# Optimization experiments

Measured on AMD Instinct MI355X. Metric: run time of the kernel, lower is better.

Reference implementation:

```python
import jax, jax.numpy as jnp
import numpy as np

N = 50000
E = 800000
IN_C, HID, OUT_C = 512, 256, 128


def gcn_conv(x, edge_index, W, b, num_nodes):
    # PyG GCNConv: add self-loops, symmetric normalization, linear-then-aggregate.
    h = x @ W  # [N, out]
    src = jnp.concatenate([edge_index[0], jnp.arange(num_nodes)])
    dst = jnp.concatenate([edge_index[1], jnp.arange(num_nodes)])
    ones = jnp.ones(src.shape[0], dtype=x.dtype)
    deg = jax.ops.segment_sum(ones, dst, num_segments=num_nodes)  # in-degree incl. self-loop
    dinv = jax.lax.rsqrt(deg)  # deg >= 1 thanks to self-loops
    norm = dinv[src] * dinv[dst]  # [E+N]
    msg = h[src] * norm[:, None]  # gather + scale
    out = jax.ops.segment_sum(msg, dst, num_segments=num_nodes)  # scatter-add
    return out + b


def setup_inputs() -> dict:
    key = jax.random.key(0)
    k_x, k_e, k_w1, k_b1, k_w2, k_b2 = jax.random.split(key, 6)
    x = jax.random.normal(k_x, (N, IN_C), dtype=jnp.float32)
    edge_index = jax.random.randint(k_e, (2, E), 0, N, dtype=jnp.int64)
    s1 = 1.0 / np.sqrt(IN_C)
    s2 = 1.0 / np.sqrt(HID)
    W1 = jax.random.uniform(k_w1, (IN_C, HID), jnp.float32, -s1, s1)
    b1 = jax.random.uniform(k_b1, (HID,), jnp.float32, -s1, s1)
    W2 = jax.random.uniform(k_w2, (HID, OUT_C), jnp.float32, -s2, s2)
    b2 = jax.random.uniform(k_b2, (OUT_C,), jnp.float32, -s2, s2)
    return {"x": x, "edge_index": edge_index, "W1": W1, "b1": b1, "W2": W2, "b2": b2}


def reference(x, edge_index, W1, b1, W2, b2):
    h = gcn_conv(x, edge_index, W1, b1, N)
    h = jax.nn.relu(h)
    # dropout in eval mode == identity
    return gcn_conv(h, edge_index, W2, b2, N)
```

## Files before the change

### kernel.cpp

```cpp
#include <hip/hip_runtime.h>
#include <stdint.h>

typedef __bf16 bf16_t;
typedef bf16_t bf16x8 __attribute__((ext_vector_type(8)));
typedef bf16_t bf16x4 __attribute__((ext_vector_type(4)));
typedef bf16_t bf16x2 __attribute__((ext_vector_type(2)));
typedef float  f32x4  __attribute__((ext_vector_type(4)));

#define IN_C 512
#define HID  256
#define OUTC 128

__global__ void k_detect(const void* __restrict__ ei, int* __restrict__ flag, int n_nodes) {
  if (blockIdx.x == 0 && threadIdx.x == 0) {
    const long long* p = (const long long*)ei;
    int ok = 1;
    for (int i = 0; i < 64; ++i) {
      long long v = p[i];
      if (v < 0 || v >= n_nodes) ok = 0;
    }
    *flag = ok;
  }
}

__global__ void k_decode_hist(const void* __restrict__ ei, const int* __restrict__ flag,
                              int* __restrict__ srcI, int* __restrict__ dstI,
                              int* __restrict__ cnt, int E) {
  int e = blockIdx.x * blockDim.x + threadIdx.x;
  if (e >= E) return;
  int s, d;
  if (*flag) {
    const long long* p = (const long long*)ei;
    s = (int)p[e];
    d = (int)p[(size_t)E + e];
  } else {
    const int* p = (const int*)ei;
    s = p[e];
    d = p[E + e];
  }
  srcI[e] = s;
  dstI[e] = d;
  atomicAdd(&cnt[d], 1);
}

__global__ void k_dinv(const int* __restrict__ cnt, float* __restrict__ dinv, int n) {
  int i = blockIdx.x * blockDim.x + threadIdx.x;
  if (i < n) dinv[i] = rsqrtf((float)cnt[i] + 1.0f);
}

__global__ void k_scan1(const int* __restrict__ cnt, int* __restrict__ ex,
                        int* __restrict__ part, int n) {
  __shared__ int sh[256];
  int i = blockIdx.x * 256 + threadIdx.x;
  int v = (i < n) ? cnt[i] : 0;
  sh[threadIdx.x] = v;
  __syncthreads();
  int val = v;
  for (int off = 1; off < 256; off <<= 1) {
    int t = (threadIdx.x >= off) ? sh[threadIdx.x - off] : 0;
    __syncthreads();
    val += t;
    sh[threadIdx.x] = val;
    __syncthreads();
  }
  if (i < n) ex[i] = val - v;
  if (threadIdx.x == 255) part[blockIdx.x] = val;
}

__global__ void k_scan2(int* __restrict__ part, int nb) {
  __shared__ int sh[256];
  int v = (threadIdx.x < nb) ? part[threadIdx.x] : 0;
  sh[threadIdx.x] = v;
  __syncthreads();
  int val = v;
  for (int off = 1; off < 256; off <<= 1) {
    int t = (threadIdx.x >= off) ? sh[threadIdx.x - off] : 0;
    __syncthreads();
    val += t;
    sh[threadIdx.x] = val;
    __syncthreads();
  }
  if (threadIdx.x < nb) part[threadIdx.x] = val - v;
}

__global__ void k_scan3(int* __restrict__ rs, const int* __restrict__ part,
                        int* __restrict__ cur, int n, int Etot) {
  int i = blockIdx.x * 256 + threadIdx.x;
  if (i < n) {
    int r = rs[i] + part[blockIdx.x];
    rs[i] = r;
    cur[i] = r;
  }
  if (i == 0) rs[n] = Etot;
}

__global__ void k_fill(const int* __restrict__ srcI, const int* __restrict__ dstI,
                       int* __restrict__ cur, int* __restrict__ csr, int E) {
  int e = blockIdx.x * blockDim.x + threadIdx.x;
  if (e >= E) return;
  int p = atomicAdd(&cur[dstI[e]], 1);
  csr[p] = srcI[e];
}

__global__ void k_convx(const float* __restrict__ x, bf16_t* __restrict__ Xb,
                        int n, int mpad) {
  int t = blockIdx.x * blockDim.x + threadIdx.x;
  int r = t >> 6, c8 = t & 63;
  if (r >= mpad) return;
  bf16x8 o;
  if (r < n) {
    const float4* px = (const float4*)(x + (size_t)r * IN_C);
    float4 a = px[c8 * 2];
    float4 b = px[c8 * 2 + 1];
    o[0] = (bf16_t)a.x; o[1] = (bf16_t)a.y; o[2] = (bf16_t)a.z; o[3] = (bf16_t)a.w;
    o[4] = (bf16_t)b.x; o[5] = (bf16_t)b.y; o[6] = (bf16_t)b.z; o[7] = (bf16_t)b.w;
  } else {
    for (int i = 0; i < 8; ++i) o[i] = (bf16_t)0.0f;
  }
  *(bf16x8*)(Xb + (size_t)r * IN_C + c8 * 8) = o;
}

__global__ void k_transpose(const float* __restrict__ W, bf16_t* __restrict__ Wt,
                            int K, int Ncols) {
  int t = blockIdx.x * blockDim.x + threadIdx.x;
  if (t >= K * Ncols) return;
  int k = t / Ncols, nn = t % Ncols;
  Wt[(size_t)nn * K + k] = (bf16_t)W[t];
}

__global__ __launch_bounds__(256, 2) void k_gemm(const bf16_t* __restrict__ A,
                                                 const bf16_t* __restrict__ Bt,
                                                 bf16_t* __restrict__ C,
                                                 int Kdim, int Ncols) {
  __shared__ bf16_t As[128 * 40];
  __shared__ bf16_t Bs[128 * 40];
  const int bm = blockIdx.x, bn = blockIdx.y;
  const int tid = threadIdx.x;
  const int wave = tid >> 6, lane = tid & 63;
  const int wm = (wave >> 1) * 64, wn = (wave & 1) * 64;
  const int quad = lane >> 4, l16 = lane & 15;
  const int seg = tid & 3;

  f32x4 acc[4][4];
  for (int i = 0; i < 4; ++i)
    for (int j = 0; j < 4; ++j)
      for (int r = 0; r < 4; ++r) acc[i][j][r] = 0.0f;

  for (int kk = 0; kk < Kdim; kk += 32) {
#pragma unroll
    for (int s = 0; s < 2; ++s) {
      int row = s * 64 + (tid >> 2);
      bf16x8 va = *(const bf16x8*)(A + (size_t)(bm * 128 + row) * Kdim + kk + seg * 8);
      *(bf16x8*)(&As[row * 40 + seg * 8]) = va;
      bf16x8 vb = *(const bf16x8*)(Bt + (size_t)(bn * 128 + row) * Kdim + kk + seg * 8);
      *(bf16x8*)(&Bs[row * 40 + seg * 8]) = vb;
    }
    __syncthreads();
    bf16x8 af[4], bfr[4];
#pragma unroll
    for (int i = 0; i < 4; ++i)
      af[i] = *(const bf16x8*)(&As[(wm + i * 16 + l16) * 40 + quad * 8]);
#pragma unroll
    for (int j = 0; j < 4; ++j)
      bfr[j] = *(const bf16x8*)(&Bs[(wn + j * 16 + l16) * 40 + quad * 8]);
#pragma unroll
    for (int i = 0; i < 4; ++i)
#pragma unroll
      for (int j = 0; j < 4; ++j)
        acc[i][j] = __builtin_amdgcn_mfma_f32_16x16x32_bf16(af[i], bfr[j], acc[i][j], 0, 0, 0);
    __syncthreads();
  }

#pragma unroll
  for (int i = 0; i < 4; ++i) {
#pragma unroll
    for (int j = 0; j < 4; ++j) {
      int col = bn * 128 + wn + j * 16 + l16;
      int row0 = bm * 128 + wm + i * 16 + quad * 4;
#pragma unroll
      for (int r = 0; r < 4; ++r)
        C[(size_t)(row0 + r) * Ncols + col] = (bf16_t)acc[i][j][r];
    }
  }
}

__global__ void k_agg_l1(const bf16_t* __restrict__ H, const int* __restrict__ rs,
                         const int* __restrict__ csr, const float* __restrict__ dinv,
                         const float* __restrict__ b1, bf16_t* __restrict__ R,
                         int n, int mpad) {
  int d = blockIdx.x * 4 + (threadIdx.x >> 6);
  if (d >= mpad) return;
  int lane = threadIdx.x & 63;
  if (d >= n) {
    bf16x4 z;
    z[0] = (bf16_t)0.0f; z[1] = (bf16_t)0.0f; z[2] = (bf16_t)0.0f; z[3] = (bf16_t)0.0f;
    *(bf16x4*)(R + (size_t)d * HID + lane * 4) = z;
    return;
  }
  int e0 = rs[d], e1 = rs[d + 1];
  float a0 = 0.f, a1 = 0.f, a2 = 0.f, a3 = 0.f;
  float c0 = 0.f, c1 = 0.f, c2 = 0.f, c3 = 0.f;
  int e = e0;
  for (; e + 2 <= e1; e += 2) {
    int s0 = csr[e], s1 = csr[e + 1];
    float w0 = dinv[s0], w1 = dinv[s1];
    bf16x4 h0 = *(const bf16x4*)(H + (size_t)s0 * HID + lane * 4);
    bf16x4 h1 = *(const bf16x4*)(H + (size_t)s1 * HID + lane * 4);
    a0 += w0 * (float)h0[0]; a1 += w0 * (float)h0[1];
    a2 += w0 * (float)h0[2]; a3 += w0 * (float)h0[3];
    c0 += w1 * (float)h1[0]; c1 += w1 * (float)h1[1];
    c2 += w1 * (float)h1[2]; c3 += w1 * (float)h1[3];
  }
  if (e < e1) {
    int s0 = csr[e];
    float w0 = dinv[s0];
    bf16x4 h0 = *(const bf16x4*)(H + (size_t)s0 * HID + lane * 4);
    a0 += w0 * (float)h0[0]; a1 += w0 * (float)h0[1];
    a2 += w0 * (float)h0[2]; a3 += w0 * (float)h0[3];
  }
  a0 += c0; a1 += c1; a2 += c2; a3 += c3;
  float dd = dinv[d];
  float dv2 = dd * dd;
  bf16x4 hs = *(const bf16x4*)(H + (size_t)d * HID + lane * 4);
  float4 bb = ((const float4*)b1)[lane];
  float v0 = fmaxf(a0 * dd + dv2 * (float)hs[0] + bb.x, 0.f);
  float v1 = fmaxf(a1 * dd + dv2 * (float)hs[1] + bb.y, 0.f);
  float v2 = fmaxf(a2 * dd + dv2 * (float)hs[2] + bb.z, 0.f);
  float v3 = fmaxf(a3 * dd + dv2 * (float)hs[3] + bb.w, 0.f);
  bf16x4 o;
  o[0] = (bf16_t)v0; o[1] = (bf16_t)v1; o[2] = (bf16_t)v2; o[3] = (bf16_t)v3;
  *(bf16x4*)(R + (size_t)d * HID + lane * 4) = o;
}

__global__ void k_agg_l2(const bf16_t* __restrict__ H, const int* __restrict__ rs,
                         const int* __restrict__ csr, const float* __restrict__ dinv,
                         const float* __restrict__ b2, float* __restrict__ out, int n) {
  int d = blockIdx.x * 4 + (threadIdx.x >> 6);
  if (d >= n) return;
  int lane = threadIdx.x & 63;
  int e0 = rs[d], e1 = rs[d + 1];
  float a0 = 0.f, a1 = 0.f, c0 = 0.f, c1 = 0.f;
  int e = e0;
  for (; e + 2 <= e1; e += 2) {
    int s0 = csr[e], s1 = csr[e + 1];
    float w0 = dinv[s0], w1 = dinv[s1];
    bf16x2 h0 = *(const bf16x2*)(H + (size_t)s0 * OUTC + lane * 2);
    bf16x2 h1 = *(const bf16x2*)(H + (size_t)s1 * OUTC + lane * 2);
    a0 += w0 * (float)h0[0]; a1 += w0 * (float)h0[1];
    c0 += w1 * (float)h1[0]; c1 += w1 * (float)h1[1];
  }
  if (e < e1) {
    int s0 = csr[e];
    float w0 = dinv[s0];
    bf16x2 h0 = *(const bf16x2*)(H + (size_t)s0 * OUTC + lane * 2);
    a0 += w0 * (float)h0[0]; a1 += w0 * (float)h0[1];
  }
  a0 += c0; a1 += c1;
  float dd = dinv[d];
  float dv2 = dd * dd;
  bf16x2 hs = *(const bf16x2*)(H + (size_t)d * OUTC + lane * 2);
  float2 bb = ((const float2*)b2)[lane];
  float2 o;
  o.x = a0 * dd + dv2 * (float)hs[0] + bb.x;
  o.y = a1 * dd + dv2 * (float)hs[1] + bb.y;
  ((float2*)(out + (size_t)d * OUTC))[lane] = o;
}

extern "C" void kernel_launch(void* const* d_in, const int* in_sizes, int n_in,
                              void* d_out, int out_size, void* d_ws, size_t ws_size,
                              hipStream_t stream) {
  const float* x  = (const float*)d_in[0];
  const void*  ei = d_in[1];
  const float* W1 = (const float*)d_in[2];
  const float* b1 = (const float*)d_in[3];
  const float* W2 = (const float*)d_in[4];
  const float* b2 = (const float*)d_in[5];

  const int n = in_sizes[0] / IN_C;
  const int E = in_sizes[1] / 2;
  const int mpad = (n + 127) & ~127;

  char* w = (char*)d_ws;
  size_t off = 0;
  auto alloc = [&](size_t bytes) -> void* {
    void* p = w + off;
    off = (off + bytes + 255) & ~(size_t)255;
    return p;
  };

  int*    flag = (int*)alloc(4);
  int*    srcI = (int*)alloc((size_t)E * 4);
  int*    dstI = (int*)alloc((size_t)E * 4);
  int*    cnt  = (int*)alloc((size_t)n * 4);
  float*  dinv = (float*)alloc((size_t)n * 4);
  int*    rs   = (int*)alloc((size_t)(n + 1) * 4);
  int*    cur  = (int*)alloc((size_t)n * 4);
  int*    part = (int*)alloc(1024);
  int*    csr  = (int*)alloc((size_t)E * 4);
  bf16_t* Xb   = (bf16_t*)alloc((size_t)mpad * IN_C * 2);
  bf16_t* W1t  = (bf16_t*)alloc((size_t)HID * IN_C * 2);
  bf16_t* H1b  = (bf16_t*)alloc((size_t)mpad * HID * 2);
  bf16_t* R1b  = (bf16_t*)alloc((size_t)mpad * HID * 2);
  bf16_t* W2t  = (bf16_t*)alloc((size_t)OUTC * HID * 2);
  bf16_t* H2b  = (bf16_t*)alloc((size_t)mpad * OUTC * 2);
  (void)ws_size; (void)n_in; (void)out_size;

  const int nb = (n + 255) / 256;

  hipMemsetAsync(cnt, 0, (size_t)n * 4, stream);
  k_detect<<<1, 64, 0, stream>>>(ei, flag, n);
  k_decode_hist<<<(E + 255) / 256, 256, 0, stream>>>(ei, flag, srcI, dstI, cnt, E);
  k_dinv<<<nb, 256, 0, stream>>>(cnt, dinv, n);
  k_scan1<<<nb, 256, 0, stream>>>(cnt, rs, part, n);
  k_scan2<<<1, 256, 0, stream>>>(part, nb);
  k_scan3<<<nb, 256, 0, stream>>>(rs, part, cur, n, E);
  k_fill<<<(E + 255) / 256, 256, 0, stream>>>(srcI, dstI, cur, csr, E);

  k_convx<<<(mpad * 64 + 255) / 256, 256, 0, stream>>>(x, Xb, n, mpad);
  k_transpose<<<(IN_C * HID + 255) / 256, 256, 0, stream>>>(W1, W1t, IN_C, HID);
  k_transpose<<<(HID * OUTC + 255) / 256, 256, 0, stream>>>(W2, W2t, HID, OUTC);

  k_gemm<<<dim3(mpad / 128, HID / 128), 256, 0, stream>>>(Xb, W1t, H1b, IN_C, HID);
  k_agg_l1<<<(mpad + 3) / 4, 256, 0, stream>>>(H1b, rs, csr, dinv, b1, R1b, n, mpad);
  k_gemm<<<dim3(mpad / 128, OUTC / 128), 256, 0, stream>>>(R1b, W2t, H2b, HID, OUTC);
  k_agg_l2<<<(n + 3) / 4, 256, 0, stream>>>(H2b, rs, csr, dinv, b2, (float*)d_out, n);
}
```

Baseline: 421.7 us.

## Fuse preprocessing kernels, store edge weights in CSR, unroll aggregation by eight

Merges the x conversion, both weight transposes, the count zeroing and the format detection into one prep kernel. The histogram kernel no longer writes decoded src/dst arrays, and the dinv computation moves into the first scan kernel. The fill kernel re-decodes edges and stores (src, dinv[src]) pairs, which removes the dependent dinv lookup during aggregation. Both aggregation kernels now issue eight gathers at once into four accumulator sets for more memory-level parallelism, at the cost of a larger CSR array and more registers.

```diff
diff --git a/kernel.cpp b/kernel.cpp
--- a/kernel.cpp
+++ b/kernel.cpp
@@ -11,21 +11,114 @@
 #define HID  256
 #define OUTC 128
 
-__global__ void k_detect(const void* __restrict__ ei, int* __restrict__ flag, int n_nodes) {
-  if (blockIdx.x == 0 && threadIdx.x == 0) {
+__global__ void k_prep(const float* __restrict__ x, const float* __restrict__ W1,
+                       const float* __restrict__ W2, const void* __restrict__ ei,
+                       int* __restrict__ flag, int* __restrict__ cnt,
+                       bf16_t* __restrict__ Xb, bf16_t* __restrict__ W1t,
+                       bf16_t* __restrict__ W2t, int n, int mpad) {
+  int t = blockIdx.x * blockDim.x + threadIdx.x;
+  const int NC = mpad * 64;
+  if (t < NC) {
+    int r = t >> 6, c8 = t & 63;
+    bf16x8 o;
+    if (r < n) {
+      const float4* px = (const float4*)(x + (size_t)r * IN_C);
+      float4 a = px[c8 * 2];
+      float4 b = px[c8 * 2 + 1];
+      o[0] = (bf16_t)a.x; o[1] = (bf16_t)a.y; o[2] = (bf16_t)a.z; o[3] = (bf16_t)a.w;
+      o[4] = (bf16_t)b.x; o[5] = (bf16_t)b.y; o[6] = (bf16_t)b.z; o[7] = (bf16_t)b.w;
+    } else {
+      for (int i = 0; i < 8; ++i) o[i] = (bf16_t)0.0f;
+    }
+    *(bf16x8*)(Xb + (size_t)r * IN_C + c8 * 8) = o;
+    return;
+  }
+  int u = t - NC;
+  if (u < IN_C * HID) {
+    W1t[(size_t)(u & 255) * IN_C + (u >> 8)] = (bf16_t)W1[u];
+    return;
+  }
+  u -= IN_C * HID;
+  if (u < HID * OUTC) {
+    W2t[(size_t)(u & 127) * HID + (u >> 7)] = (bf16_t)W2[u];
+    return;
+  }
+  u -= HID * OUTC;
+  if (u < n) {
+    cnt[u] = 0;
+    return;
+  }
+  if (u == n) {
     const long long* p = (const long long*)ei;
     int ok = 1;
     for (int i = 0; i < 64; ++i) {
       long long v = p[i];
-      if (v < 0 || v >= n_nodes) ok = 0;
+      if (v < 0 || v >= n) ok = 0;
     }
     *flag = ok;
   }
 }
 
-__global__ void k_decode_hist(const void* __restrict__ ei, const int* __restrict__ flag,
-                              int* __restrict__ srcI, int* __restrict__ dstI,
-                              int* __restrict__ cnt, int E) {
+__global__ void k_hist(const void* __restrict__ ei, const int* __restrict__ flag,
+                       int* __restrict__ cnt, int E) {
+  int e = blockIdx.x * blockDim.x + threadIdx.x;
+  if (e >= E) return;
+  int d;
+  if (*flag) d = (int)((const long long*)ei)[(size_t)E + e];
+  else       d = ((const int*)ei)[E + e];
+  atomicAdd(&cnt[d], 1);
+}
+
+__global__ void k_scan1(const int* __restrict__ cnt, int* __restrict__ ex,
+                        int* __restrict__ part, float* __restrict__ dinv, int n) {
+  __shared__ int sh[256];
+  int i = blockIdx.x * 256 + threadIdx.x;
+  int v = (i < n) ? cnt[i] : 0;
+  if (i < n) dinv[i] = rsqrtf((float)v + 1.0f);
+  sh[threadIdx.x] = v;
+  __syncthreads();
+  int val = v;
+  for (int off = 1; off < 256; off <<= 1) {
+    int t = (threadIdx.x >= off) ? sh[threadIdx.x - off] : 0;
+    __syncthreads();
+    val += t;
+    sh[threadIdx.x] = val;
+    __syncthreads();
+  }
+  if (i < n) ex[i] = val - v;
+  if (threadIdx.x == 255) part[blockIdx.x] = val;
+}
+
+__global__ void k_scan2(int* __restrict__ part, int nb) {
+  __shared__ int sh[256];
+  int v = (threadIdx.x < nb) ? part[threadIdx.x] : 0;
+  sh[threadIdx.x] = v;
+  __syncthreads();
+  int val = v;
+  for (int off = 1; off < 256; off <<= 1) {
+    int t = (threadIdx.x >= off) ? sh[threadIdx.x - off] : 0;
+    __syncthreads();
+    val += t;
+    sh[threadIdx.x] = val;
+    __syncthreads();
+  }
+  if (threadIdx.x < nb) part[threadIdx.x] = val - v;
+}
+
+__global__ void k_scan3(int* __restrict__ rs, const int* __restrict__ part,
+                        int* __restrict__ cur, int n, int Etot) {
+  int i = blockIdx.x * 256 + threadIdx.x;
+  if (i < n) {
+    int r = rs[i] + part[blockIdx.x];
+    rs[i] = r;
+    cur[i] = r;
+  }
+  if (i == 0) rs[n] = Etot;
+}
+
+__global__ void k_fill(const void* __restrict__ ei, const int* __restrict__ flag,
+                       int* __restrict__ cur, int2* __restrict__ csrw,
+                       const float* __restrict__ dinv, int E) {
   int e = blockIdx.x * blockDim.x + threadIdx.x;
   if (e >= E) return;
   int s, d;
@@ -38,94 +131,11 @@
     s = p[e];
     d = p[E + e];
   }
-  srcI[e] = s;
-  dstI[e] = d;
-  atomicAdd(&cnt[d], 1);
-}
-
-__global__ void k_dinv(const int* __restrict__ cnt, float* __restrict__ dinv, int n) {
-  int i = blockIdx.x * blockDim.x + threadIdx.x;
-  if (i < n) dinv[i] = rsqrtf((float)cnt[i] + 1.0f);
-}
-
-__global__ void k_scan1(const int* __restrict__ cnt, int* __restrict__ ex,
-                        int* __restrict__ part, int n) {
-  __shared__ int sh[256];
-  int i = blockIdx.x * 256 + threadIdx.x;
-  int v = (i < n) ? cnt[i] : 0;
-  sh[threadIdx.x] = v;
-  __syncthreads();
-  int val = v;
-  for (int off = 1; off < 256; off <<= 1) {
-    int t = (threadIdx.x >= off) ? sh[threadIdx.x - off] : 0;
-    __syncthreads();
-    val += t;
-    sh[threadIdx.x] = val;
-    __syncthreads();
-  }
-  if (i < n) ex[i] = val - v;
-  if (threadIdx.x == 255) part[blockIdx.x] = val;
-}
-
-__global__ void k_scan2(int* __restrict__ part, int nb) {
-  __shared__ int sh[256];
-  int v = (threadIdx.x < nb) ? part[threadIdx.x] : 0;
-  sh[threadIdx.x] = v;
-  __syncthreads();
-  int val = v;
-  for (int off = 1; off < 256; off <<= 1) {
-    int t = (threadIdx.x >= off) ? sh[threadIdx.x - off] : 0;
-    __syncthreads();
-    val += t;
-    sh[threadIdx.x] = val;
-    __syncthreads();
-  }
-  if (threadIdx.x < nb) part[threadIdx.x] = val - v;
-}
-
-__global__ void k_scan3(int* __restrict__ rs, const int* __restrict__ part,
-                        int* __restrict__ cur, int n, int Etot) {
-  int i = blockIdx.x * 256 + threadIdx.x;
-  if (i < n) {
-    int r = rs[i] + part[blockIdx.x];
-    rs[i] = r;
-    cur[i] = r;
-  }
-  if (i == 0) rs[n] = Etot;
-}
-
-__global__ void k_fill(const int* __restrict__ srcI, const int* __restrict__ dstI,
-                       int* __restrict__ cur, int* __restrict__ csr, int E) {
-  int e = blockIdx.x * blockDim.x + threadIdx.x;
-  if (e >= E) return;
-  int p = atomicAdd(&cur[dstI[e]], 1);
-  csr[p] = srcI[e];
-}
-
-__global__ void k_convx(const float* __restrict__ x, bf16_t* __restrict__ Xb,
-                        int n, int mpad) {
-  int t = blockIdx.x * blockDim.x + threadIdx.x;
-  int r = t >> 6, c8 = t & 63;
-  if (r >= mpad) return;
-  bf16x8 o;
-  if (r < n) {
-    const float4* px = (const float4*)(x + (size_t)r * IN_C);
-    float4 a = px[c8 * 2];
-    float4 b = px[c8 * 2 + 1];
-    o[0] = (bf16_t)a.x; o[1] = (bf16_t)a.y; o[2] = (bf16_t)a.z; o[3] = (bf16_t)a.w;
-    o[4] = (bf16_t)b.x; o[5] = (bf16_t)b.y; o[6] = (bf16_t)b.z; o[7] = (bf16_t)b.w;
-  } else {
-    for (int i = 0; i < 8; ++i) o[i] = (bf16_t)0.0f;
-  }
-  *(bf16x8*)(Xb + (size_t)r * IN_C + c8 * 8) = o;
-}
-
-__global__ void k_transpose(const float* __restrict__ W, bf16_t* __restrict__ Wt,
-                            int K, int Ncols) {
-  int t = blockIdx.x * blockDim.x + threadIdx.x;
-  if (t >= K * Ncols) return;
-  int k = t / Ncols, nn = t % Ncols;
-  Wt[(size_t)nn * K + k] = (bf16_t)W[t];
+  int pos = atomicAdd(&cur[d], 1);
+  int2 v;
+  v.x = s;
+  v.y = __float_as_int(dinv[s]);
+  csrw[pos] = v;
 }
 
 __global__ __launch_bounds__(256, 2) void k_gemm(const bf16_t* __restrict__ A,
@@ -185,7 +195,7 @@
 }
 
 __global__ void k_agg_l1(const bf16_t* __restrict__ H, const int* __restrict__ rs,
-                         const int* __restrict__ csr, const float* __restrict__ dinv,
+                         const int2* __restrict__ csrw, const float* __restrict__ dinv,
                          const float* __restrict__ b1, bf16_t* __restrict__ R,
                          int n, int mpad) {
   int d = blockIdx.x * 4 + (threadIdx.x >> 6);
@@ -198,31 +208,40 @@
     return;
   }
   int e0 = rs[d], e1 = rs[d + 1];
-  float a0 = 0.f, a1 = 0.f, a2 = 0.f, a3 = 0.f;
-  float c0 = 0.f, c1 = 0.f, c2 = 0.f, c3 = 0.f;
+  float acc[4][4];
+  for (int k = 0; k < 4; ++k)
+    for (int c = 0; c < 4; ++c) acc[k][c] = 0.f;
   int e = e0;
-  for (; e + 2 <= e1; e += 2) {
-    int s0 = csr[e], s1 = csr[e + 1];
-    float w0 = dinv[s0], w1 = dinv[s1];
-    bf16x4 h0 = *(const bf16x4*)(H + (size_t)s0 * HID + lane * 4);
-    bf16x4 h1 = *(const bf16x4*)(H + (size_t)s1 * HID + lane * 4);
-    a0 += w0 * (float)h0[0]; a1 += w0 * (float)h0[1];
-    a2 += w0 * (float)h0[2]; a3 += w0 * (float)h0[3];
-    c0 += w1 * (float)h1[0]; c1 += w1 * (float)h1[1];
-    c2 += w1 * (float)h1[2]; c3 += w1 * (float)h1[3];
-  }
-  if (e < e1) {
-    int s0 = csr[e];
-    float w0 = dinv[s0];
-    bf16x4 h0 = *(const bf16x4*)(H + (size_t)s0 * HID + lane * 4);
-    a0 += w0 * (float)h0[0]; a1 += w0 * (float)h0[1];
-    a2 += w0 * (float)h0[2]; a3 += w0 * (float)h0[3];
-  }
-  a0 += c0; a1 += c1; a2 += c2; a3 += c3;
+  for (; e + 8 <= e1; e += 8) {
+    int2 cw[8];
+    bf16x4 h[8];
+#pragma unroll
+    for (int u = 0; u < 8; ++u) cw[u] = csrw[e + u];
+#pragma unroll
+    for (int u = 0; u < 8; ++u)
+      h[u] = *(const bf16x4*)(H + (size_t)cw[u].x * HID + lane * 4);
+#pragma unroll
+    for (int u = 0; u < 8; ++u) {
+      float w = __int_as_float(cw[u].y);
+#pragma unroll
+      for (int c = 0; c < 4; ++c) acc[u & 3][c] += w * (float)h[u][c];
+    }
+  }
+  for (; e < e1; ++e) {
+    int2 cw = csrw[e];
+    float w = __int_as_float(cw.y);
+    bf16x4 hx = *(const bf16x4*)(H + (size_t)cw.x * HID + lane * 4);
+#pragma unroll
+    for (int c = 0; c < 4; ++c) acc[0][c] += w * (float)hx[c];
+  }
   float dd = dinv[d];
   float dv2 = dd * dd;
   bf16x4 hs = *(const bf16x4*)(H + (size_t)d * HID + lane * 4);
   float4 bb = ((const float4*)b1)[lane];
+  float a0 = (acc[0][0] + acc[1][0]) + (acc[2][0] + acc[3][0]);
+  float a1 = (acc[0][1] + acc[1][1]) + (acc[2][1] + acc[3][1]);
+  float a2 = (acc[0][2] + acc[1][2]) + (acc[2][2] + acc[3][2]);
+  float a3 = (acc[0][3] + acc[1][3]) + (acc[2][3] + acc[3][3]);
   float v0 = fmaxf(a0 * dd + dv2 * (float)hs[0] + bb.x, 0.f);
   float v1 = fmaxf(a1 * dd + dv2 * (float)hs[1] + bb.y, 0.f);
   float v2 = fmaxf(a2 * dd + dv2 * (float)hs[2] + bb.z, 0.f);
@@ -233,29 +252,39 @@
 }
 
 __global__ void k_agg_l2(const bf16_t* __restrict__ H, const int* __restrict__ rs,
-                         const int* __restrict__ csr, const float* __restrict__ dinv,
+                         const int2* __restrict__ csrw, const float* __restrict__ dinv,
                          const float* __restrict__ b2, float* __restrict__ out, int n) {
   int d = blockIdx.x * 4 + (threadIdx.x >> 6);
   if (d >= n) return;
   int lane = threadIdx.x & 63;
   int e0 = rs[d], e1 = rs[d + 1];
-  float a0 = 0.f, a1 = 0.f, c0 = 0.f, c1 = 0.f;
+  float acc[4][2];
+  for (int k = 0; k < 4; ++k) { acc[k][0] = 0.f; acc[k][1] = 0.f; }
   int e = e0;
-  for (; e + 2 <= e1; e += 2) {
-    int s0 = csr[e], s1 = csr[e + 1];
-    float w0 = dinv[s0], w1 = dinv[s1];
-    bf16x2 h0 = *(const bf16x2*)(H + (size_t)s0 * OUTC + lane * 2);
-    bf16x2 h1 = *(const bf16x2*)(H + (size_t)s1 * OUTC + lane * 2);
-    a0 += w0 * (float)h0[0]; a1 += w0 * (float)h0[1];
-    c0 += w1 * (float)h1[0]; c1 += w1 * (float)h1[1];
-  }
-  if (e < e1) {
-    int s0 = csr[e];
-    float w0 = dinv[s0];
-    bf16x2 h0 = *(const bf16x2*)(H + (size_t)s0 * OUTC + lane * 2);
-    a0 += w0 * (float)h0[0]; a1 += w0 * (float)h0[1];
-  }
-  a0 += c0; a1 += c1;
+  for (; e + 8 <= e1; e += 8) {
+    int2 cw[8];
+    bf16x2 h[8];
+#pragma unroll
+    for (int u = 0; u < 8; ++u) cw[u] = csrw[e + u];
+#pragma unroll
+    for (int u = 0; u < 8; ++u)
+      h[u] = *(const bf16x2*)(H + (size_t)cw[u].x * OUTC + lane * 2);
+#pragma unroll
+    for (int u = 0; u < 8; ++u) {
+      float w = __int_as_float(cw[u].y);
+      acc[u & 3][0] += w * (float)h[u][0];
+      acc[u & 3][1] += w * (float)h[u][1];
+    }
+  }
+  for (; e < e1; ++e) {
+    int2 cw = csrw[e];
+    float w = __int_as_float(cw.y);
+    bf16x2 hx = *(const bf16x2*)(H + (size_t)cw.x * OUTC + lane * 2);
+    acc[0][0] += w * (float)hx[0];
+    acc[0][1] += w * (float)hx[1];
+  }
+  float a0 = (acc[0][0] + acc[1][0]) + (acc[2][0] + acc[3][0]);
+  float a1 = (acc[0][1] + acc[1][1]) + (acc[2][1] + acc[3][1]);
   float dd = dinv[d];
   float dv2 = dd * dd;
   bf16x2 hs = *(const bf16x2*)(H + (size_t)d * OUTC + lane * 2);
@@ -289,39 +318,33 @@
   };
 
   int*    flag = (int*)alloc(4);
-  int*    srcI = (int*)alloc((size_t)E * 4);
-  int*    dstI = (int*)alloc((size_t)E * 4);
   int*    cnt  = (int*)alloc((size_t)n * 4);
   float*  dinv = (float*)alloc((size_t)n * 4);
   int*    rs   = (int*)alloc((size_t)(n + 1) * 4);
   int*    cur  = (int*)alloc((size_t)n * 4);
   int*    part = (int*)alloc(1024);
-  int*    csr  = (int*)alloc((size_t)E * 4);
+  int2*   csrw = (int2*)alloc((size_t)E * 8);
   bf16_t* Xb   = (bf16_t*)alloc((size_t)mpad * IN_C * 2);
   bf16_t* W1t  = (bf16_t*)alloc((size_t)HID * IN_C * 2);
+  bf16_t* W2t  = (bf16_t*)alloc((size_t)OUTC * HID * 2);
   bf16_t* H1b  = (bf16_t*)alloc((size_t)mpad * HID * 2);
   bf16_t* R1b  = (bf16_t*)alloc((size_t)mpad * HID * 2);
-  bf16_t* W2t  = (bf16_t*)alloc((size_t)OUTC * HID * 2);
   bf16_t* H2b  = (bf16_t*)alloc((size_t)mpad * OUTC * 2);
   (void)ws_size; (void)n_in; (void)out_size;
 
   const int nb = (n + 255) / 256;
-
-  hipMemsetAsync(cnt, 0, (size_t)n * 4, stream);
-  k_detect<<<1, 64, 0, stream>>>(ei, flag, n);
-  k_decode_hist<<<(E + 255) / 256, 256, 0, stream>>>(ei, flag, srcI, dstI, cnt, E);
-  k_dinv<<<nb, 256, 0, stream>>>(cnt, dinv, n);
-  k_scan1<<<nb, 256, 0, stream>>>(cnt, rs, part, n);
+  const int prepT = mpad * 64 + IN_C * HID + HID * OUTC + n + 1;
+
+  k_prep<<<(prepT + 255) / 256, 256, 0, stream>>>(x, W1, W2, ei, flag, cnt,
+                                                  Xb, W1t, W2t, n, mpad);
+  k_hist<<<(E + 255) / 256, 256, 0, stream>>>(ei, flag, cnt, E);
+  k_scan1<<<nb, 256, 0, stream>>>(cnt, rs, part, dinv, n);
   k_scan2<<<1, 256, 0, stream>>>(part, nb);
   k_scan3<<<nb, 256, 0, stream>>>(rs, part, cur, n, E);
-  k_fill<<<(E + 255) / 256, 256, 0, stream>>>(srcI, dstI, cur, csr, E);
-
-  k_convx<<<(mpad * 64 + 255) / 256, 256, 0, stream>>>(x, Xb, n, mpad);
-  k_transpose<<<(IN_C * HID + 255) / 256, 256, 0, stream>>>(W1, W1t, IN_C, HID);
-  k_transpose<<<(HID * OUTC + 255) / 256, 256, 0, stream>>>(W2, W2t, HID, OUTC);
+  k_fill<<<(E + 255) / 256, 256, 0, stream>>>(ei, flag, cur, csrw, dinv, E);
 
   k_gemm<<<dim3(mpad / 128, HID / 128), 256, 0, stream>>>(Xb, W1t, H1b, IN_C, HID);
-  k_agg_l1<<<(mpad + 3) / 4, 256, 0, stream>>>(H1b, rs, csr, dinv, b1, R1b, n, mpad);
+  k_agg_l1<<<(mpad + 3) / 4, 256, 0, stream>>>(H1b, rs, csrw, dinv, b1, R1b, n, mpad);
   k_gemm<<<dim3(mpad / 128, OUTC / 128), 256, 0, stream>>>(R1b, W2t, H2b, HID, OUTC);
-  k_agg_l2<<<(n + 3) / 4, 256, 0, stream>>>(H2b, rs, csr, dinv, b2, (float*)d_out, n);
-}
+  k_agg_l2<<<(n + 3) / 4, 256, 0, stream>>>(H2b, rs, csrw, dinv, b2, (float*)d_out, n);
+}
```

Result: faster. 398.3 us (-5.6%).
